# Kernel tuning notes

Hardware: AMD Instinct MI355X
Metric: run time of the kernel (lower is better)

The kernel has to match this reference:

```python
import jax, jax.numpy as jnp
import numpy as np

# Inner model dims (concrete MLP standing in for the wrapped keras model)
D_IN, HID, D_OUT = 1024, 2048, 10
POP, STD = 40, 0.1
S1 = D_IN * HID          # end of W1
S2 = S1 + HID            # end of b1
S3 = S2 + HID * D_OUT    # end of W2
N_PARAMS = S3 + D_OUT    # 2,119,690


def _flatten_weights(W1, b1, W2, b2):
    # tf.concat([reshape(w, [-1]) for w in trainable_weights])
    return jnp.concatenate([W1.reshape(-1), b1, W2.reshape(-1), b2])


def _mse_loss(flat_w, x, y):
    # expand_flat_trainable_weights + forward + compiled_loss (MSE)
    W1 = flat_w[:S1].reshape(D_IN, HID)
    b1 = flat_w[S1:S2]
    W2 = flat_w[S2:S3].reshape(HID, D_OUT)
    b2 = flat_w[S3:]
    pred = jax.nn.relu(x @ W1 + b1) @ W2 + b2
    return jnp.mean((pred - y) ** 2)


def _centered_ranks(t):
    # compute_centered_ranks: argsort-based ranks in [0, n), centered to [-0.5, 0.5]
    flat = t.reshape(-1)
    n = flat.shape[0]
    ranks = jnp.zeros((n,), jnp.float32).at[jnp.argsort(flat)].set(
        jnp.arange(n, dtype=jnp.float32))
    return (ranks / (n - 1) - 0.5).reshape(t.shape)


def setup_inputs() -> dict:
    key = jax.random.key(0)
    ks = jax.random.split(key, 5)
    return {
        "x": jax.random.normal(ks[0], (256, D_IN), jnp.float32),
        "y": jax.random.normal(ks[1], (256, D_OUT), jnp.float32),
        "W1": jax.random.normal(ks[2], (D_IN, HID), jnp.float32) * 0.02,
        "b1": jnp.zeros((HID,), jnp.float32),
        "W2": jax.random.normal(ks[3], (HID, D_OUT), jnp.float32) * 0.02,
        "b2": jnp.zeros((D_OUT,), jnp.float32),
        "noise": jax.random.normal(ks[4], (POP, N_PARAMS), jnp.float32),
    }


def reference(x, y, W1, b1, W2, b2, noise):
    flat_w = _flatten_weights(W1, b1, W2, b2)          # [N]
    eps = noise * STD                                   # stddev-scaled noise [POP, N]
    # parity: i even -> +1, i odd -> -1 (antithetic pairs)
    parity = jnp.array([1.0, -1.0], jnp.float32)
    perturbed = flat_w[None, None, :] + eps[:, None, :] * parity[None, :, None]  # [POP,2,N]
    # batched replacement for the pop_size*2 sequential forward passes
    losses = jax.vmap(jax.vmap(lambda w: _mse_loss(w, x, y)))(perturbed)  # [POP, 2]
    proc = _centered_ranks(losses)
    proc = proc[:, 0] - proc[:, 1]                      # [POP]
    grad = jnp.tensordot(eps, proc, axes=[[0], [0]]) / (POP * STD)  # [N]
    return grad
```

## Files before the change

kernel.cpp:

```cpp
#include <hip/hip_runtime.h>


#define NPLL 2119690LL
#define S1_  2097152
#define S2_  2099200
#define S3_  2119680

#define WS_PP   524288
#define WS_LOSS 3801088
#define WS_G    3801168
#define WS_XF   3801216
#define WW_PP   524288
#define WW_LOSS 7077888
#define WW_G    7077968
#define WW_XF   7078016
#define WW_NEED_BYTES 28836352ull

typedef _Float16 f16;
typedef __fp16   fp16x2 __attribute__((ext_vector_type(2)));
typedef _Float16 f16x2t __attribute__((ext_vector_type(2)));
typedef _Float16 f16x8 __attribute__((ext_vector_type(8)));
typedef float    f32x4 __attribute__((ext_vector_type(4)));

__device__ __forceinline__ unsigned pk2r(float a, float b, float& ra, float& rb) {
  fp16x2 h = __builtin_amdgcn_cvt_pkrtz(a, b);
  ra = a - (float)h[0];
  rb = b - (float)h[1];
  return __builtin_bit_cast(unsigned, h);
}
__device__ __forceinline__ unsigned pk2(float a, float b) {
  fp16x2 h = __builtin_amdgcn_cvt_pkrtz(a, b);
  return __builtin_bit_cast(unsigned, h);
}
__device__ __forceinline__ unsigned packh(float a, float b) {
  f16x2t v = {(f16)a, (f16)b};
  return __builtin_bit_cast(unsigned, v);
}
__device__ __forceinline__ float unpk_lo(unsigned u) {
  return (float)__builtin_bit_cast(f16, (unsigned short)(u & 0xffffu));
}
__device__ __forceinline__ float unpk_hi(unsigned u) {
  return (float)__builtin_bit_cast(f16, (unsigned short)(u >> 16));
}

__global__ __launch_bounds__(256) void k_xsplit(const float* __restrict__ x,
                                                f16* __restrict__ xf) {
  const int idx = blockIdx.x * 256 + threadIdx.x;
  const int b  = idx >> 7;
  const int k8 = idx & 127;
  const int kt = k8 >> 2, qh = k8 & 3;
  const int bblk = b >> 4, lm = b & 15;
  float4 a0 = *(const float4*)&x[(size_t)b * 1024 + k8 * 8];
  float4 a1 = *(const float4*)&x[(size_t)b * 1024 + k8 * 8 + 4];
  uint4 H;
  H.x = packh(a0.x, a0.y);
  H.y = packh(a0.z, a0.w);
  H.z = packh(a1.x, a1.y);
  H.w = packh(a1.z, a1.w);
  f16* dst = &xf[(((size_t)(kt * 16 + bblk) * 4 + qh) * 16 + lm) * 8];
  *(uint4*)dst = H;
}

__global__ __launch_bounds__(256) void k_base(const float* __restrict__ x,
                                              const float* __restrict__ W1,
                                              const float* __restrict__ b1,
                                              float* __restrict__ base) {
  constexpr int STR = 72;
  __shared__ float xsm[32 * STR];
  __shared__ float es[32 * STR];
  const int t  = threadIdx.x;
  const int j0 = blockIdx.x * 64;
  const int b0 = blockIdx.y * 32;
  const int tj = t & 15;
  const int tb = t >> 4;
  float acc[4][2] = {};
  for (int k0 = 0; k0 < 1024; k0 += 32) {
    __syncthreads();
    {
      int bb = t >> 3, kq = t & 7;
      float4 v = *(const float4*)&x[(size_t)(b0 + bb) * 1024 + k0 + kq * 4];
      int kb = kq * 4;
      xsm[(kb + 0) * STR + bb] = v.x;
      xsm[(kb + 1) * STR + bb] = v.y;
      xsm[(kb + 2) * STR + bb] = v.z;
      xsm[(kb + 3) * STR + bb] = v.w;
    }
#pragma unroll
    for (int r = 0; r < 2; ++r) {
      int idx = t + r * 256;
      int k = idx >> 4, jq = idx & 15, col = jq * 4;
      float4 v = *(const float4*)&W1[(size_t)(k0 + k) * 2048 + j0 + col];
      *(float4*)&es[k * STR + col + 4 * (col >> 5)] = v;
    }
    __syncthreads();
#pragma unroll 8
    for (int k = 0; k < 32; ++k) {
      const int ce = tj * 4;
      float4 e = *(const float4*)&es[k * STR + ce + 4 * (ce >> 5)];
      float2 a = *(const float2*)&xsm[k * STR + tb * 2];
      acc[0][0] += e.x * a.x; acc[0][1] += e.x * a.y;
      acc[1][0] += e.y * a.x; acc[1][1] += e.y * a.y;
      acc[2][0] += e.z * a.x; acc[2][1] += e.z * a.y;
      acc[3][0] += e.w * a.x; acc[3][1] += e.w * a.y;
    }
  }
#pragma unroll
  for (int jj = 0; jj < 4; ++jj) {
    int j = j0 + tj * 4 + jj;
    float bv = b1[j];
    float2 o = make_float2(acc[jj][0] + bv, acc[jj][1] + bv);
    *(float2*)&base[(size_t)j * 256 + b0 + tb * 2] = o;
  }
}

__global__ __launch_bounds__(256, 2) void k_big32(const f16* __restrict__ xf,
                                                  const float* __restrict__ noise,
                                                  const float* __restrict__ W2,
                                                  const float* __restrict__ base,
                                                  unsigned* __restrict__ ppu) {
  __shared__ __align__(16) char smem[5888];
  float* w2l = (float*)smem;
  float* e2l = w2l + 320;
  float* e1l = e2l + 320;

  const int t    = threadIdx.x;
  const int jt   = blockIdx.x, p = blockIdx.y;
  const int j0   = jt * 32;
  const int wave = t >> 6, lane = t & 63;
  const int lm   = lane & 15, qh = lane >> 4;
  const int g4   = qh * 4;
  const int bw   = wave * 64;
  const size_t pN = (size_t)p * NPLL;
  const int srow = t & 31, sq = t >> 5;
  const int wOff = srow * 40 + (sq >> 1) * 8 + (sq & 1) * 4;
  constexpr int STR16 = 40;

  f16* eA0 = (f16*)smem;
  f16* eA1 = (f16*)(smem + 2560);

  float veA[4], veB[4], veC[4], veD[4];
  f16x8 Ba[4], Bb[4];
  f32x4 acc[2][4];
#pragma unroll
  for (int a = 0; a < 2; ++a)
#pragma unroll
    for (int b = 0; b < 4; ++b) acc[a][b] = (f32x4){0.f, 0.f, 0.f, 0.f};

  const float* Ebase = noise + pN + (size_t)(sq * 4) * 2048 + j0 + srow;
  const int boff = (wave * 4) * 512 + qh * 128 + lm * 8;

#pragma unroll
  for (int d = 0; d < 4; ++d) veA[d] = Ebase[(size_t)d * 2048];
#pragma unroll
  for (int d = 0; d < 4; ++d) veB[d] = Ebase[65536 + (size_t)d * 2048];
#pragma unroll
  for (int d = 0; d < 4; ++d) veC[d] = Ebase[131072 + (size_t)d * 2048];
#pragma unroll
  for (int d = 0; d < 4; ++d) veD[d] = Ebase[196608 + (size_t)d * 2048];
#pragma unroll
  for (int nf = 0; nf < 4; ++nf)
    Ba[nf] = *(const f16x8*)&xf[boff + nf * 512];
#pragma unroll
  for (int nf = 0; nf < 4; ++nf)
    Bb[nf] = *(const f16x8*)&xf[8192 + boff + nf * 512];

#define KSTEP32(EAC, VE, BF, KS)                                               \
  do {                                                                         \
    {                     \
      uint2 H;                                                                 \
      H.x = packh(VE[0], VE[1]);                                               \
      H.y = packh(VE[2], VE[3]);                                               \
      *(uint2*)&EAC[wOff] = H;                                                 \
    }                                                                          \
    if ((KS) + 4 < 32) {                 \
      const float* En = Ebase + (size_t)((KS) + 4) * 65536;                    \
      _Pragma("unroll") for (int d = 0; d < 4; ++d)                            \
        VE[d] = En[(size_t)d * 2048];                                          \
    }                                                                          \
    asm volatile("s_waitcnt lgkmcnt(0)" ::: "memory");     \
    __builtin_amdgcn_s_barrier();                        \
    asm volatile("" ::: "memory");                                             \
    _Pragma("unroll") for (int mf = 0; mf < 2; ++mf) {                         \
      const int ra = mf * 16 + lm;                                             \
      f16x8 Ah = *(const f16x8*)&EAC[ra * STR16 + qh * 8];                     \
      _Pragma("unroll") for (int nf = 0; nf < 4; ++nf)                         \
        acc[mf][nf] = __builtin_amdgcn_mfma_f32_16x16x32_f16(Ah, BF[nf], acc[mf][nf], 0, 0, 0); \
    }                                                                          \
    if ((KS) + 2 < 32) {      \
      const f16* xn = xf + (size_t)((KS) + 2) * 8192;                          \
      _Pragma("unroll") for (int nf = 0; nf < 4; ++nf)                         \
        BF[nf] = *(const f16x8*)&xn[boff + nf * 512];                          \
    }                                                                          \
  } while (0)

  for (int ks = 0; ks < 32; ks += 4) {
    KSTEP32(eA0, veA, Ba, ks);
    KSTEP32(eA1, veB, Bb, ks + 1);
    KSTEP32(eA0, veC, Ba, ks + 2);
    KSTEP32(eA1, veD, Bb, ks + 3);
  }
#undef KSTEP32

  __syncthreads();
  for (int i = t; i < 320; i += 256) {
    w2l[i] = W2[j0 * 10 + i];
    e2l[i] = noise[pN + S2_ + (size_t)j0 * 10 + i];
  }
  if (t < 32) e1l[t] = noise[pN + S1_ + j0 + t];
  __syncthreads();

#pragma unroll 1
  for (int s = 0; s < 2; ++s) {
    const float sf = s ? -0.1f : 0.1f;
#pragma unroll 1
    for (int nf = 0; nf < 4; ++nf) {
      const int bl = bw + nf * 16 + lm;
      float ppv[10];
#pragma unroll
      for (int o = 0; o < 10; ++o) ppv[o] = 0.f;
#pragma unroll
      for (int mf = 0; mf < 2; ++mf)
#pragma unroll
        for (int r = 0; r < 4; ++r) {
          const int jl = mf * 16 + g4 + r;
          const float bs = base[(size_t)(j0 + jl) * 256 + bl];
          const float h =
              fmaxf(fmaf(sf, acc[mf][nf][r] + e1l[jl], bs), 0.f);
#pragma unroll
          for (int o = 0; o < 10; ++o)
            ppv[o] = fmaf(h, fmaf(sf, e2l[jl * 10 + o], w2l[jl * 10 + o]),
                          ppv[o]);
        }
#pragma unroll
      for (int o = 0; o < 10; ++o) {
        float v = ppv[o];
        v += __shfl_xor(v, 16, 64);
        v += __shfl_xor(v, 32, 64);
        ppv[o] = v;
      }
      if (lane < 16) {
        const size_t u0 = ((((size_t)p * 2 + s) * 64 + jt) * 256 + bl) * 5;
        ppu[u0 + 0] = packh(ppv[0], ppv[1]);
        ppu[u0 + 1] = packh(ppv[2], ppv[3]);
        ppu[u0 + 2] = packh(ppv[4], ppv[5]);
        ppu[u0 + 3] = packh(ppv[6], ppv[7]);
        ppu[u0 + 4] = packh(ppv[8], ppv[9]);
      }
    }
  }
}

__global__ __launch_bounds__(256) void k_big64(const f16* __restrict__ xf,
                                               const float* __restrict__ noise,
                                               const float* __restrict__ W2,
                                               const float* __restrict__ base,
                                               unsigned* __restrict__ ppu) {
  __shared__ __align__(16) char smem[16384];
  float* w2l = (float*)smem;
  float* e2l = w2l + 640;
  float* e1l = e2l + 640;

  const int t    = threadIdx.x;
  const int jt   = blockIdx.x, p = blockIdx.y;
  const int j0   = jt * 64;
  const int wave = t >> 6, lane = t & 63;
  const int lm   = lane & 15, qh = lane >> 4;
  const int g4   = qh * 4;
  const int bw   = wave * 64;
  const size_t pN = (size_t)p * NPLL;
  const int srow = t & 63, sq = t >> 6;
  const int sswz = (srow & 7) << 3;
  const int aswz = (lm & 7) << 3;

  f16* eA0 = (f16*)smem;
  f16* eA1 = (f16*)(smem + 8192);

  float veA[8], veB[8];
  f16x8 Ba[4], Bb[4];
  f32x4 acc[4][4];
#pragma unroll
  for (int a = 0; a < 4; ++a)
#pragma unroll
    for (int b = 0; b < 4; ++b) acc[a][b] = (f32x4){0.f, 0.f, 0.f, 0.f};

  const float* Ebase = noise + pN + (size_t)(sq * 8) * 2048 + j0 + srow;
  const int boff = (wave * 4) * 512 + qh * 128 + lm * 8;

#pragma unroll
  for (int d = 0; d < 8; ++d) veA[d] = Ebase[(size_t)d * 2048];
#pragma unroll
  for (int nf = 0; nf < 4; ++nf)
    Ba[nf] = *(const f16x8*)&xf[boff + nf * 512];
#pragma unroll
  for (int d = 0; d < 8; ++d) veB[d] = Ebase[65536 + (size_t)d * 2048];
#pragma unroll
  for (int nf = 0; nf < 4; ++nf)
    Bb[nf] = *(const f16x8*)&xf[8192 + boff + nf * 512];

#define KSTEP64(EAC, VE, BF, KS)                                               \
  do {                                                                         \
    {                                                                          \
      float r0, r1, r2, r3, r4, r5, r6, r7;                                    \
      uint4 H, L;                                                              \
      H.x = pk2r(VE[0], VE[1], r0, r1);                                        \
      H.y = pk2r(VE[2], VE[3], r2, r3);                                        \
      H.z = pk2r(VE[4], VE[5], r4, r5);                                        \
      H.w = pk2r(VE[6], VE[7], r6, r7);                                        \
      *(uint4*)&EAC[srow * 64 + ((sq * 8) ^ sswz)] = H;                        \
      L.x = pk2(r0, r1); L.y = pk2(r2, r3);                                    \
      L.z = pk2(r4, r5); L.w = pk2(r6, r7);                                    \
      *(uint4*)&EAC[srow * 64 + (((sq + 4) * 8) ^ sswz)] = L;                  \
    }                                                                          \
    if ((KS) + 2 < 32) {                                                       \
      const float* En = Ebase + (size_t)((KS) + 2) * 65536;                    \
      _Pragma("unroll") for (int d = 0; d < 8; ++d)                            \
        VE[d] = En[(size_t)d * 2048];                                          \
    }                                                                          \
    asm volatile("s_waitcnt lgkmcnt(0)" ::: "memory");                         \
    __builtin_amdgcn_s_barrier();                                              \
    asm volatile("" ::: "memory");                                             \
    _Pragma("unroll") for (int mf = 0; mf < 4; ++mf) {                         \
      const int ra = mf * 16 + lm;                                             \
      f16x8 Ah = *(const f16x8*)&EAC[ra * 64 + ((qh * 8) ^ aswz)];             \
      f16x8 Al = *(const f16x8*)&EAC[ra * 64 + (((qh + 4) * 8) ^ aswz)];       \
      _Pragma("unroll") for (int nf = 0; nf < 4; ++nf) {                       \
        acc[mf][nf] = __builtin_amdgcn_mfma_f32_16x16x32_f16(Ah, BF[nf], acc[mf][nf], 0, 0, 0); \
        acc[mf][nf] = __builtin_amdgcn_mfma_f32_16x16x32_f16(Al, BF[nf], acc[mf][nf], 0, 0, 0); \
      }                                                                        \
    }                                                                          \
    if ((KS) + 2 < 32) {                                                       \
      const f16* xn = xf + (size_t)((KS) + 2) * 8192;                          \
      _Pragma("unroll") for (int nf = 0; nf < 4; ++nf)                         \
        BF[nf] = *(const f16x8*)&xn[boff + nf * 512];                          \
    }                                                                          \
  } while (0)

  for (int ks = 0; ks < 32; ks += 2) {
    KSTEP64(eA0, veA, Ba, ks);
    KSTEP64(eA1, veB, Bb, ks + 1);
  }
#undef KSTEP64

  __syncthreads();
  for (int i = t; i < 640; i += 256) {
    w2l[i] = W2[j0 * 10 + i];
    e2l[i] = noise[pN + S2_ + (size_t)j0 * 10 + i];
  }
  if (t < 64) e1l[t] = noise[pN + S1_ + j0 + t];
  __syncthreads();

#pragma unroll 1
  for (int s = 0; s < 2; ++s) {
    const float sf = s ? -0.1f : 0.1f;
    float ppv[4][10];
#pragma unroll
    for (int nf = 0; nf < 4; ++nf)
#pragma unroll
      for (int o = 0; o < 10; ++o) ppv[nf][o] = 0.f;
#pragma unroll
    for (int mf = 0; mf < 4; ++mf)
#pragma unroll
      for (int r = 0; r < 4; ++r) {
        const int jl = mf * 16 + g4 + r;
        const float e1v = e1l[jl];
        float w2s[10];
#pragma unroll
        for (int o = 0; o < 10; ++o)
          w2s[o] = fmaf(sf, e2l[jl * 10 + o], w2l[jl * 10 + o]);
#pragma unroll
        for (int nf = 0; nf < 4; ++nf) {
          const float bs = base[(size_t)(j0 + jl) * 256 + bw + nf * 16 + lm];
          const float h = fmaxf(fmaf(sf, acc[mf][nf][r] + e1v, bs), 0.f);
#pragma unroll
          for (int o = 0; o < 10; ++o) ppv[nf][o] = fmaf(h, w2s[o], ppv[nf][o]);
        }
      }
#pragma unroll
    for (int nf = 0; nf < 4; ++nf)
#pragma unroll
      for (int o = 0; o < 10; ++o) {
        float v = ppv[nf][o];
        v += __shfl_xor(v, 16, 64);
        v += __shfl_xor(v, 32, 64);
        ppv[nf][o] = v;
      }
    if (lane < 16) {
#pragma unroll
      for (int nf = 0; nf < 4; ++nf) {
        const int bl = bw + nf * 16 + lm;
        const size_t u0 = ((((size_t)p * 2 + s) * 32 + jt) * 256 + bl) * 5;
        ppu[u0 + 0] = packh(ppv[nf][0], ppv[nf][1]);
        ppu[u0 + 1] = packh(ppv[nf][2], ppv[nf][3]);
        ppu[u0 + 2] = packh(ppv[nf][4], ppv[nf][5]);
        ppu[u0 + 3] = packh(ppv[nf][6], ppv[nf][7]);
        ppu[u0 + 4] = packh(ppv[nf][8], ppv[nf][9]);
      }
    }
  }
}

__global__ __launch_bounds__(256) void k_loss(const unsigned* __restrict__ ppu,
                                              const float* __restrict__ y,
                                              const float* __restrict__ b2,
                                              const float* __restrict__ noise,
                                              float* __restrict__ loss,
                                              int JT) {
  const int b = threadIdx.x;
  const int p = blockIdx.x >> 1, s = blockIdx.x & 1;
  const float sf = s ? -0.1f : 0.1f;
  const size_t pN = (size_t)p * NPLL;
  float pred[10];
#pragma unroll
  for (int o = 0; o < 10; ++o) pred[o] = b2[o] + sf * noise[pN + S3_ + o];
  for (int jt = 0; jt < JT; ++jt) {
    const size_t u0 = ((((size_t)p * 2 + s) * JT + jt) * 256 + b) * 5;
#pragma unroll
    for (int q = 0; q < 5; ++q) {
      unsigned u = ppu[u0 + q];
      pred[2 * q]     += unpk_lo(u);
      pred[2 * q + 1] += unpk_hi(u);
    }
  }
  float e = 0.f;
#pragma unroll
  for (int o = 0; o < 10; ++o) {
    float d = pred[o] - y[b * 10 + o];
    e += d * d;
  }
  __shared__ float red[256];
  red[b] = e;
  __syncthreads();
  for (int st = 128; st > 0; st >>= 1) {
    if (b < st) red[b] += red[b + st];
    __syncthreads();
  }
  if (b == 0) loss[blockIdx.x] = red[0] * (1.0f / 2560.0f);
}

__global__ void k_rank(const float* __restrict__ loss, float* __restrict__ g) {
  __shared__ float ls[80];
  __shared__ float rk[80];
  const int t = threadIdx.x;
  if (t < 80) ls[t] = loss[t];
  __syncthreads();
  if (t < 80) {
    float li = ls[t];
    int r = 0;
    for (int j = 0; j < 80; ++j) {
      float lj = ls[j];
      r += (lj < li) || (lj == li && j < t);
    }
    rk[t] = (float)r;
  }
  __syncthreads();
  if (t < 40) g[t] = (rk[2 * t] - rk[2 * t + 1]) * (1.0f / (79.0f * 40.0f));
}

__global__ __launch_bounds__(256) void k_grad(const float* __restrict__ noise,
                                              const float* __restrict__ g,
                                              float* __restrict__ out) {
  __shared__ float gg[40];
  const int t = threadIdx.x;
  if (t < 40) gg[t] = g[t];
  __syncthreads();
  const long long NH = NPLL / 2;
  long long idx = (long long)blockIdx.x * 256 + t;
  if (idx >= NH) return;
  float2 a = make_float2(0.f, 0.f);
#pragma unroll 8
  for (int p = 0; p < 40; ++p) {
    float2 v = *(const float2*)&noise[(size_t)p * NPLL + idx * 2];
    a.x += v.x * gg[p];
    a.y += v.y * gg[p];
  }
  *(float2*)&out[idx * 2] = a;
}

extern "C" void kernel_launch(void* const* d_in, const int* in_sizes, int n_in,
                              void* d_out, int out_size, void* d_ws, size_t ws_size,
                              hipStream_t stream) {
  const float* x     = (const float*)d_in[0];
  const float* y     = (const float*)d_in[1];
  const float* W1    = (const float*)d_in[2];
  const float* b1    = (const float*)d_in[3];
  const float* W2    = (const float*)d_in[4];
  const float* b2    = (const float*)d_in[5];
  const float* noise = (const float*)d_in[6];
  float* out  = (float*)d_out;
  float* ws   = (float*)d_ws;
  float* base = ws;

  const bool wide = (ws_size >= WW_NEED_BYTES);
  unsigned* ppu = (unsigned*)(ws + (wide ? WW_PP : WS_PP));
  float* loss = ws + (wide ? WW_LOSS : WS_LOSS);
  float* g    = ws + (wide ? WW_G : WS_G);
  f16* xf     = (f16*)(ws + (wide ? WW_XF : WS_XF));

  k_xsplit<<<128, 256, 0, stream>>>(x, xf);
  k_base<<<dim3(32, 8), 256, 0, stream>>>(x, W1, b1, base);
  if (wide)
    k_big32<<<dim3(64, 40), 256, 0, stream>>>(xf, noise, W2, base, ppu);
  else
    k_big64<<<dim3(32, 40), 256, 0, stream>>>(xf, noise, W2, base, ppu);
  k_loss<<<80, 256, 0, stream>>>(ppu, y, b2, noise, loss, wide ? 64 : 32);
  k_rank<<<1, 128, 0, stream>>>(loss, g);
  k_grad<<<4141, 256, 0, stream>>>(noise, g, out);
}
```

Before: 330.7 us.

## Widen big kernel to 64-column tiles with 512-thread blocks sharing B fragments

Replaces the 32-column, 256-thread wide-path kernel with a 64-column, 512-thread version. Wave pairs split the column tile and share the same x fragments, which halves the number of blocks and doubles reuse of the staged noise tile per barrier. Partial outputs keep the 64-slot layout so the loss kernel is unchanged. The cost is larger blocks with more barrier participants, and register pressure under launch_bounds(512,2) may reduce occupancy.

```diff
diff --git a/kernel.cpp b/kernel.cpp
--- a/kernel.cpp
+++ b/kernel.cpp
@@ -113,30 +113,31 @@
   }
 }
 
-__global__ __launch_bounds__(256, 2) void k_big32(const f16* __restrict__ xf,
-                                                  const float* __restrict__ noise,
-                                                  const float* __restrict__ W2,
-                                                  const float* __restrict__ base,
-                                                  unsigned* __restrict__ ppu) {
-  __shared__ __align__(16) char smem[5888];
+__global__ __launch_bounds__(512, 2) void k_bigw(const f16* __restrict__ xf,
+                                                 const float* __restrict__ noise,
+                                                 const float* __restrict__ W2,
+                                                 const float* __restrict__ base,
+                                                 unsigned* __restrict__ ppu) {
+  __shared__ __align__(16) char smem[10240];
   float* w2l = (float*)smem;
-  float* e2l = w2l + 320;
-  float* e1l = e2l + 320;
+  float* e2l = w2l + 640;
+  float* e1l = e2l + 640;
 
   const int t    = threadIdx.x;
   const int jt   = blockIdx.x, p = blockIdx.y;
-  const int j0   = jt * 32;
+  const int j0   = jt * 64;
   const int wave = t >> 6, lane = t & 63;
   const int lm   = lane & 15, qh = lane >> 4;
   const int g4   = qh * 4;
-  const int bw   = wave * 64;
+  const int jw   = (wave & 1) * 32;
+  const int bq   = wave >> 1, bw = bq * 64;
   const size_t pN = (size_t)p * NPLL;
-  const int srow = t & 31, sq = t >> 5;
-  const int wOff = srow * 40 + (sq >> 1) * 8 + (sq & 1) * 4;
+  const int srow = lane, sk = wave;
+  const int wOff = srow * 40 + sk * 4;
   constexpr int STR16 = 40;
 
   f16* eA0 = (f16*)smem;
-  f16* eA1 = (f16*)(smem + 2560);
+  f16* eA1 = (f16*)(smem + 5120);
 
   float veA[4], veB[4], veC[4], veD[4];
   f16x8 Ba[4], Bb[4];
@@ -146,8 +147,8 @@
 #pragma unroll
     for (int b = 0; b < 4; ++b) acc[a][b] = (f32x4){0.f, 0.f, 0.f, 0.f};
 
-  const float* Ebase = noise + pN + (size_t)(sq * 4) * 2048 + j0 + srow;
-  const int boff = (wave * 4) * 512 + qh * 128 + lm * 8;
+  const float* Ebase = noise + pN + (size_t)(sk * 4) * 2048 + j0 + srow;
+  const int boff = (bq * 4) * 512 + qh * 128 + lm * 8;
 
 #pragma unroll
   for (int d = 0; d < 4; ++d) veA[d] = Ebase[(size_t)d * 2048];
@@ -164,7 +165,7 @@
   for (int nf = 0; nf < 4; ++nf)
     Bb[nf] = *(const f16x8*)&xf[8192 + boff + nf * 512];
 
-#define KSTEP32(EAC, VE, BF, KS)                                               \
+#define KSTEP(EAC, VE, BF, KS)                                                 \
   do {                                                                         \
     {                     \
       uint2 H;                                                                 \
@@ -181,7 +182,7 @@
     __builtin_amdgcn_s_barrier();                        \
     asm volatile("" ::: "memory");                                             \
     _Pragma("unroll") for (int mf = 0; mf < 2; ++mf) {                         \
-      const int ra = mf * 16 + lm;                                             \
+      const int ra = jw + mf * 16 + lm;                                        \
       f16x8 Ah = *(const f16x8*)&EAC[ra * STR16 + qh * 8];                     \
       _Pragma("unroll") for (int nf = 0; nf < 4; ++nf)                         \
         acc[mf][nf] = __builtin_amdgcn_mfma_f32_16x16x32_f16(Ah, BF[nf], acc[mf][nf], 0, 0, 0); \
@@ -194,19 +195,19 @@
   } while (0)
 
   for (int ks = 0; ks < 32; ks += 4) {
-    KSTEP32(eA0, veA, Ba, ks);
-    KSTEP32(eA1, veB, Bb, ks + 1);
-    KSTEP32(eA0, veC, Ba, ks + 2);
-    KSTEP32(eA1, veD, Bb, ks + 3);
-  }
-#undef KSTEP32
-
-  __syncthreads();
-  for (int i = t; i < 320; i += 256) {
+    KSTEP(eA0, veA, Ba, ks);
+    KSTEP(eA1, veB, Bb, ks + 1);
+    KSTEP(eA0, veC, Ba, ks + 2);
+    KSTEP(eA1, veD, Bb, ks + 3);
+  }
+#undef KSTEP
+
+  __syncthreads();
+  for (int i = t; i < 640; i += 512) {
     w2l[i] = W2[j0 * 10 + i];
     e2l[i] = noise[pN + S2_ + (size_t)j0 * 10 + i];
   }
-  if (t < 32) e1l[t] = noise[pN + S1_ + j0 + t];
+  if (t < 64) e1l[t] = noise[pN + S1_ + j0 + t];
   __syncthreads();
 
 #pragma unroll 1
@@ -222,7 +223,7 @@
       for (int mf = 0; mf < 2; ++mf)
 #pragma unroll
         for (int r = 0; r < 4; ++r) {
-          const int jl = mf * 16 + g4 + r;
+          const int jl = jw + mf * 16 + g4 + r;
           const float bs = base[(size_t)(j0 + jl) * 256 + bl];
           const float h =
               fmaxf(fmaf(sf, acc[mf][nf][r] + e1l[jl], bs), 0.f);
@@ -239,7 +240,8 @@
         ppv[o] = v;
       }
       if (lane < 16) {
-        const size_t u0 = ((((size_t)p * 2 + s) * 64 + jt) * 256 + bl) * 5;
+        const size_t u0 =
+            ((((size_t)p * 2 + s) * 64 + (jt * 2 + (wave & 1))) * 256 + bl) * 5;
         ppu[u0 + 0] = packh(ppv[0], ppv[1]);
         ppu[u0 + 1] = packh(ppv[2], ppv[3]);
         ppu[u0 + 2] = packh(ppv[4], ppv[5]);
@@ -499,7 +501,7 @@
   k_xsplit<<<128, 256, 0, stream>>>(x, xf);
   k_base<<<dim3(32, 8), 256, 0, stream>>>(x, W1, b1, base);
   if (wide)
-    k_big32<<<dim3(64, 40), 256, 0, stream>>>(xf, noise, W2, base, ppu);
+    k_bigw<<<dim3(32, 40), 512, 0, stream>>>(xf, noise, W2, base, ppu);
   else
     k_big64<<<dim3(32, 40), 256, 0, stream>>>(xf, noise, W2, base, ppu);
   k_loss<<<80, 256, 0, stream>>>(ppu, y, b2, noise, loss, wide ? 64 : 32);
```

Result: faster. 318.2 us (-3.8%).
